# Optimization experiments

Hardware: AMD Instinct MI355X
Metric: run time of the kernel (lower is better)

## Reference

```python
import math
import jax, jax.numpy as jnp
import numpy as np

B, H, N, M, DQ, DV, P = 8, 16, 1024, 1024, 64, 64, 64
N_HEADS = 16


def setup_inputs() -> dict:
    key = jax.random.key(0)
    ks = jax.random.split(key, 6)
    return {
        "queries": jax.random.normal(ks[0], (B, H, N, DQ), dtype=jnp.float32),
        "keys": jax.random.normal(ks[1], (B, H, M, DQ), dtype=jnp.float32),
        "values": jax.random.normal(ks[2], (B, H, M, DV), dtype=jnp.float32),
        # learned relative positional encoding table, leading broadcast dim of 1
        "pos_enc": jax.random.normal(ks[3], (1, N, M, P), dtype=jnp.float32) * 0.02,
        # nn.Linear(P, 1): weight (1,P) stored flat as (P,), bias (1,)
        "w_pos": jax.random.normal(ks[4], (P,), dtype=jnp.float32) * (1.0 / math.sqrt(P)),
        "b_pos": jnp.zeros((1,), dtype=jnp.float32),
        "query_sequence_pad_length": N,
        "key_value_sequence_pad_length": M,
    }


def reference(queries, keys, values, pos_enc, w_pos, b_pos,
              query_sequence_pad_length, key_value_sequence_pad_length):
    n = query_sequence_pad_length
    m = key_value_sequence_pad_length
    Bsz, Hn = queries.shape[0], queries.shape[1]

    # source: tmp = keys if N == M else queries
    tmp = keys if queries.shape[2] == keys.shape[2] else queries
    # raw scores, scaled by 1/sqrt(n_heads) (faithful to source)
    scores = jnp.einsum('bhnd,bhmd->bhnm', tmp, keys) / math.sqrt(N_HEADS)  # (B,H,n,m)

    # map_pos(scores[...,None] + pos) with Linear(P,1) is affine, so it equals
    # scores * sum(w) + (pos . w + b)  — exact algebraic rewrite avoiding the
    # (B,H,n,m,P) broadcast blowup.
    pos_bias = jnp.einsum('nmp,p->nm', pos_enc[0, :n, :m, :], w_pos) + b_pos[0]  # (n,m)
    attn = scores * jnp.sum(w_pos) + pos_bias  # (B,H,n,m)

    attn = attn.reshape(Bsz * Hn, n, m)
    q = queries.reshape(Bsz * Hn, n, queries.shape[-1])
    k = keys.reshape(Bsz * Hn, m, keys.shape[-1])
    v = values.reshape(Bsz * Hn, m, values.shape[-1])
    return (attn, q, k, v)
```

## Files before the change

kernel.cpp:

```cpp
#include <hip/hip_runtime.h>
#include <hip/hip_bf16.h>

typedef __attribute__((ext_vector_type(8))) short short8;
typedef __attribute__((ext_vector_type(4))) float f32x4;

constexpr int N = 1024, M = 1024, D = 64, BH = 128;
constexpr size_t ATTN_ELEMS = (size_t)BH * N * M;
constexpr size_t QKV_ELEMS  = (size_t)BH * N * D;
constexpr int PB_BLOCKS = 2048;
constexpr int COPY_BLOCKS_PER = 256;
constexpr int BGROUP = 8;
constexpr int BR = 32, BC = 256;

__device__ __forceinline__ short f2b(float x) {
    __hip_bfloat16 h = __float2bfloat16(x);
    return *reinterpret_cast<short*>(&h);
}

__global__ void prep_kernel(const float* __restrict__ q, const float* __restrict__ k,
                            const float* __restrict__ v, const float* __restrict__ pos,
                            const float* __restrict__ w, const float* __restrict__ b,
                            float* __restrict__ pb, float* __restrict__ scale_p,
                            float* __restrict__ qout, float* __restrict__ kout,
                            float* __restrict__ vout, int ncopy) {
    const int bid = blockIdx.x, tid = threadIdx.x;
    if (bid < PB_BLOCKS) {
        const int lane16 = tid & 15;
        const f32x4 w4 = ((const f32x4*)w)[lane16];
        const float bias = b[0];
        const int group = (bid * 256 + tid) >> 4;
        const int ngroups = (PB_BLOCKS * 256) >> 4;
        for (int pair = group; pair < N * M; pair += ngroups) {
            f32x4 p = __builtin_nontemporal_load((const f32x4*)pos + (size_t)pair * 16 + lane16);
            float s = p[0]*w4[0] + p[1]*w4[1] + p[2]*w4[2] + p[3]*w4[3];
            s += __shfl_xor(s, 1);
            s += __shfl_xor(s, 2);
            s += __shfl_xor(s, 4);
            s += __shfl_xor(s, 8);
            if (lane16 == 0) pb[pair] = s + bias;
        }
    } else if (bid < PB_BLOCKS + ncopy) {
        const int cid = bid - PB_BLOCKS;
        const int which = cid >> 8, lid = cid & 255;
        const f32x4* __restrict__ src = (which == 0) ? (const f32x4*)q
                                      : (which == 1) ? (const f32x4*)k : (const f32x4*)v;
        f32x4* __restrict__ dst = (which == 0) ? (f32x4*)qout
                                : (which == 1) ? (f32x4*)kout : (f32x4*)vout;
        const int nel4 = (int)(QKV_ELEMS / 4);
        for (int i = lid * 256 + tid; i < nel4; i += COPY_BLOCKS_PER * 256) {
            f32x4 x = __builtin_nontemporal_load(src + i);
            __builtin_nontemporal_store(x, dst + i);
        }
    } else {
        if (tid < 64) {
            float val = w[tid];
#pragma unroll
            for (int o = 32; o > 0; o >>= 1) val += __shfl_down(val, o);
            if (tid == 0) scale_p[0] = val * 0.25f;
        }
    }
}

__launch_bounds__(256)
__global__ void attn_kernel(const float* __restrict__ keys, const float* __restrict__ pb,
                            const float* __restrict__ scale_p, float* __restrict__ out) {
    __shared__ short lK[(BR + BC) * 64];
    const int pos = blockIdx.x;
    const int tr = pos >> 2, tc = pos & 3;
    const int batch0 = blockIdx.y * BGROUP;
    const int tid = threadIdx.x;
    const float scale = scale_p[0];

    const int lane = tid & 63, wv = tid >> 6;
    const int wr = wv >> 1, wc = wv & 1;
    const int frow = lane & 15;
    const int kslot = lane >> 4;

    const int orow = tr * BR + wr * 16 + (lane >> 4) * 4;
    const int ocol = tc * BC + wc * 128 + (lane & 15);

    f32x4 pf[8];
#pragma unroll
    for (int j = 0; j < 8; j++)
#pragma unroll
        for (int r = 0; r < 4; r++)
            pf[j][r] = pb[(size_t)(orow + r) * M + (ocol + j * 16)];

    for (int t = 0; t < BGROUP; ++t) {
        const float* __restrict__ Kb = keys + (size_t)(batch0 + t) * N * D;

#pragma unroll
        for (int it = 0; it < 9; ++it) {
            const int slot = it * 256 + tid;
            const int row = slot >> 3, s16 = slot & 7;
            const int gr = (row < BR) ? (tr * BR + row) : (tc * BC + (row - BR));
            const f32x4* src = (const f32x4*)(Kb + (size_t)gr * D + s16 * 8);
            f32x4 x0 = src[0], x1 = src[1];
            short8 pk;
#pragma unroll
            for (int e = 0; e < 4; e++) { pk[e] = f2b(x0[e]); pk[4 + e] = f2b(x1[e]); }
            *(short8*)&lK[row * 64 + (s16 ^ (row & 7)) * 8] = pk;
        }
        __syncthreads();

        f32x4 acc[8] = {};
#pragma unroll
        for (int h = 0; h < 2; ++h) {
            const int ra = wr * 16 + frow;
            short8 a = *(const short8*)&lK[ra * 64 + ((h * 4 + kslot) ^ (ra & 7)) * 8];
#pragma unroll
            for (int j = 0; j < 8; j++) {
                const int rb = BR + wc * 128 + j * 16 + frow;
                short8 bf = *(const short8*)&lK[rb * 64 + ((h * 4 + kslot) ^ (rb & 7)) * 8];
                acc[j] = __builtin_amdgcn_mfma_f32_16x16x32_bf16(a, bf, acc[j], 0, 0, 0);
            }
        }

        const size_t obase = (size_t)(batch0 + t) * N * M;
#pragma unroll
        for (int j = 0; j < 8; j++)
#pragma unroll
            for (int r = 0; r < 4; r++) {
                out[obase + (size_t)(orow + r) * M + (ocol + j * 16)]
                    = acc[j][r] * scale + pf[j][r];
            }
        __syncthreads();
    }
}

extern "C" void kernel_launch(void* const* d_in, const int* in_sizes, int n_in,
                              void* d_out, int out_size, void* d_ws, size_t ws_size,
                              hipStream_t stream) {
    const float* queries = (const float*)d_in[0];
    const float* keys    = (const float*)d_in[1];
    const float* values  = (const float*)d_in[2];
    const float* pos_enc = (const float*)d_in[3];
    const float* w_pos   = (const float*)d_in[4];
    const float* b_pos   = (const float*)d_in[5];

    float* out  = (float*)d_out;
    float* qout = out + ATTN_ELEMS;
    float* kout = qout + QKV_ELEMS;
    float* vout = kout + QKV_ELEMS;

    const bool use_ws = ws_size >= ((size_t)N * M + 16) * sizeof(float);
    const int npos = (N / BR) * (M / BC);

    if (use_ws) {
        float* pb      = (float*)d_ws;
        float* scale_p = pb + (size_t)N * M;
        const int ncopy = 3 * COPY_BLOCKS_PER;
        prep_kernel<<<dim3(PB_BLOCKS + ncopy + 1), dim3(256), 0, stream>>>(
            queries, keys, values, pos_enc, w_pos, b_pos, pb, scale_p,
            qout, kout, vout, ncopy);
        attn_kernel<<<dim3(npos, BH / BGROUP), dim3(256), 0, stream>>>(keys, pb, scale_p, out);
    } else {
        float* pb      = qout;
        float* scale_p = pb + (size_t)N * M;
        prep_kernel<<<dim3(PB_BLOCKS + 1), dim3(256), 0, stream>>>(
            queries, keys, values, pos_enc, w_pos, b_pos, pb, scale_p,
            qout, kout, vout, 0);
        attn_kernel<<<dim3(npos, BH / BGROUP), dim3(256), 0, stream>>>(keys, pb, scale_p, out);
        hipMemcpyAsync(qout, queries, QKV_ELEMS * sizeof(float), hipMemcpyDeviceToDevice, stream);
        hipMemcpyAsync(kout, keys,    QKV_ELEMS * sizeof(float), hipMemcpyDeviceToDevice, stream);
        hipMemcpyAsync(vout, values,  QKV_ELEMS * sizeof(float), hipMemcpyDeviceToDevice, stream);
    }
}
```

Measured before the change: 256.3 us.

## Pre-convert keys to swizzled bf16 in prep kernel and load via global_load_lds

Adds a key-conversion stage to the prep kernel that writes keys as bf16 in a pre-swizzled layout into workspace. The attention kernel then loads tiles directly into LDS with global_load_lds instead of loading fp32, converting and storing through registers. This halves the bytes read for the repeated K tile loads and removes per-tile conversion work. The cost is an extra 16 MB workspace write plus read, and the fallback path now writes the bf16 keys into the output region, which may overlap the q/k/v output buffers.

```diff
diff --git a/kernel.cpp b/kernel.cpp
--- a/kernel.cpp
+++ b/kernel.cpp
@@ -3,11 +3,13 @@
 
 typedef __attribute__((ext_vector_type(8))) short short8;
 typedef __attribute__((ext_vector_type(4))) float f32x4;
+typedef unsigned int u32;
 
 constexpr int N = 1024, M = 1024, D = 64, BH = 128;
 constexpr size_t ATTN_ELEMS = (size_t)BH * N * M;
 constexpr size_t QKV_ELEMS  = (size_t)BH * N * D;
 constexpr int PB_BLOCKS = 2048;
+constexpr int KCONV_BLOCKS = 512;
 constexpr int COPY_BLOCKS_PER = 256;
 constexpr int BGROUP = 8;
 constexpr int BR = 32, BC = 256;
@@ -17,10 +19,17 @@
     return *reinterpret_cast<short*>(&h);
 }
 
+__device__ __forceinline__ void gl_lds16(const void* g, void* l) {
+    __builtin_amdgcn_global_load_lds(
+        (const __attribute__((address_space(1))) u32*)g,
+        (__attribute__((address_space(3))) u32*)l, 16, 0, 0);
+}
+
 __global__ void prep_kernel(const float* __restrict__ q, const float* __restrict__ k,
                             const float* __restrict__ v, const float* __restrict__ pos,
                             const float* __restrict__ w, const float* __restrict__ b,
-                            float* __restrict__ pb, float* __restrict__ scale_p,
+                            float* __restrict__ pb, short* __restrict__ kbf,
+                            float* __restrict__ scale_p,
                             float* __restrict__ qout, float* __restrict__ kout,
                             float* __restrict__ vout, int ncopy) {
     const int bid = blockIdx.x, tid = threadIdx.x;
@@ -39,8 +48,20 @@
             s += __shfl_xor(s, 8);
             if (lane16 == 0) pb[pair] = s + bias;
         }
-    } else if (bid < PB_BLOCKS + ncopy) {
+    } else if (bid < PB_BLOCKS + KCONV_BLOCKS) {
         const int cid = bid - PB_BLOCKS;
+        const int total_slots = BH * N * 8;
+        for (int gs = cid * 256 + tid; gs < total_slots; gs += KCONV_BLOCKS * 256) {
+            const int qs = gs & 7, gr = (gs >> 3) & (N - 1), bb = gs >> 13;
+            const float* src = k + ((size_t)bb * N + gr) * D + (qs ^ (gr & 7)) * 8;
+            f32x4 x0 = ((const f32x4*)src)[0], x1 = ((const f32x4*)src)[1];
+            short8 pk;
+#pragma unroll
+            for (int e = 0; e < 4; e++) { pk[e] = f2b(x0[e]); pk[4 + e] = f2b(x1[e]); }
+            *(short8*)&kbf[(size_t)gs * 8] = pk;
+        }
+    } else if (bid < PB_BLOCKS + KCONV_BLOCKS + ncopy) {
+        const int cid = bid - PB_BLOCKS - KCONV_BLOCKS;
         const int which = cid >> 8, lid = cid & 255;
         const f32x4* __restrict__ src = (which == 0) ? (const f32x4*)q
                                       : (which == 1) ? (const f32x4*)k : (const f32x4*)v;
@@ -62,7 +83,7 @@
 }
 
 __launch_bounds__(256)
-__global__ void attn_kernel(const float* __restrict__ keys, const float* __restrict__ pb,
+__global__ void attn_kernel(const short* __restrict__ kbf, const float* __restrict__ pb,
                             const float* __restrict__ scale_p, float* __restrict__ out) {
     __shared__ short lK[(BR + BC) * 64];
     const int pos = blockIdx.x;
@@ -87,19 +108,14 @@
             pf[j][r] = pb[(size_t)(orow + r) * M + (ocol + j * 16)];
 
     for (int t = 0; t < BGROUP; ++t) {
-        const float* __restrict__ Kb = keys + (size_t)(batch0 + t) * N * D;
+        const short* __restrict__ Kb = kbf + (size_t)(batch0 + t) * N * 64;
 
 #pragma unroll
         for (int it = 0; it < 9; ++it) {
             const int slot = it * 256 + tid;
-            const int row = slot >> 3, s16 = slot & 7;
+            const int row = slot >> 3, qs = slot & 7;
             const int gr = (row < BR) ? (tr * BR + row) : (tc * BC + (row - BR));
-            const f32x4* src = (const f32x4*)(Kb + (size_t)gr * D + s16 * 8);
-            f32x4 x0 = src[0], x1 = src[1];
-            short8 pk;
-#pragma unroll
-            for (int e = 0; e < 4; e++) { pk[e] = f2b(x0[e]); pk[4 + e] = f2b(x1[e]); }
-            *(short8*)&lK[row * 64 + (s16 ^ (row & 7)) * 8] = pk;
+            gl_lds16(Kb + (size_t)gr * 64 + qs * 8, &lK[slot * 8]);
         }
         __syncthreads();
 
@@ -143,24 +159,27 @@
     float* kout = qout + QKV_ELEMS;
     float* vout = kout + QKV_ELEMS;
 
-    const bool use_ws = ws_size >= ((size_t)N * M + 16) * sizeof(float);
+    const size_t need_ws = ((size_t)N * M + 16) * sizeof(float)
+                         + (size_t)BH * N * 64 * sizeof(short);
     const int npos = (N / BR) * (M / BC);
 
-    if (use_ws) {
+    if (ws_size >= need_ws) {
         float* pb      = (float*)d_ws;
         float* scale_p = pb + (size_t)N * M;
+        short* kbf     = (short*)(scale_p + 16);
         const int ncopy = 3 * COPY_BLOCKS_PER;
-        prep_kernel<<<dim3(PB_BLOCKS + ncopy + 1), dim3(256), 0, stream>>>(
-            queries, keys, values, pos_enc, w_pos, b_pos, pb, scale_p,
+        prep_kernel<<<dim3(PB_BLOCKS + KCONV_BLOCKS + ncopy + 1), dim3(256), 0, stream>>>(
+            queries, keys, values, pos_enc, w_pos, b_pos, pb, kbf, scale_p,
             qout, kout, vout, ncopy);
-        attn_kernel<<<dim3(npos, BH / BGROUP), dim3(256), 0, stream>>>(keys, pb, scale_p, out);
+        attn_kernel<<<dim3(npos, BH / BGROUP), dim3(256), 0, stream>>>(kbf, pb, scale_p, out);
     } else {
         float* pb      = qout;
         float* scale_p = pb + (size_t)N * M;
-        prep_kernel<<<dim3(PB_BLOCKS + 1), dim3(256), 0, stream>>>(
-            queries, keys, values, pos_enc, w_pos, b_pos, pb, scale_p,
+        short* kbf     = (short*)(scale_p + 16);
+        prep_kernel<<<dim3(PB_BLOCKS + KCONV_BLOCKS + 1), dim3(256), 0, stream>>>(
+            queries, keys, values, pos_enc, w_pos, b_pos, pb, kbf, scale_p,
             qout, kout, vout, 0);
-        attn_kernel<<<dim3(npos, BH / BGROUP), dim3(256), 0, stream>>>(keys, pb, scale_p, out);
+        attn_kernel<<<dim3(npos, BH / BGROUP), dim3(256), 0, stream>>>(kbf, pb, scale_p, out);
         hipMemcpyAsync(qout, queries, QKV_ELEMS * sizeof(float), hipMemcpyDeviceToDevice, stream);
         hipMemcpyAsync(kout, keys,    QKV_ELEMS * sizeof(float), hipMemcpyDeviceToDevice, stream);
         hipMemcpyAsync(vout, values,  QKV_ELEMS * sizeof(float), hipMemcpyDeviceToDevice, stream);
```

Result: faster. 206.2 us (-19.6%).
